# Performance work log

Measured on AMD Instinct MI355X. Metric: run time of the kernel, lower is better.

Reference implementation:

```python
import jax, jax.numpy as jnp
import numpy as np

EPS = 1e-3  # Keras LayerNormalization default epsilon


def _lstm(x, mask, Wk, Wr, b):
    """Masked Keras-style LSTM, return_sequences=True, zero initial state.
    x: [B,T,F], mask: [B,T] bool, Wk: [F,4U], Wr: [U,4U], b: [4U].
    Gate order i,f,g,o (Keras). Masked steps carry previous h,c through."""
    B, T, _ = x.shape
    U = Wr.shape[0]
    # precompute input projections for all timesteps: [B,T,4U]
    zx = jnp.einsum('btf,fg->btg', x, Wk) + b

    def step(carry, inp):
        h, c = carry
        zx_t, m_t = inp  # [B,4U], [B]
        z = zx_t + h @ Wr
        i, f, g, o = jnp.split(z, 4, axis=-1)
        c_new = jax.nn.sigmoid(f) * c + jax.nn.sigmoid(i) * jnp.tanh(g)
        h_new = jax.nn.sigmoid(o) * jnp.tanh(c_new)
        m = m_t[:, None]
        h = jnp.where(m, h_new, h)
        c = jnp.where(m, c_new, c)
        return (h, c), h

    init = (jnp.zeros((B, U), x.dtype), jnp.zeros((B, U), x.dtype))
    _, hs = jax.lax.scan(step, init, (jnp.swapaxes(zx, 0, 1), mask.T))
    return jnp.swapaxes(hs, 0, 1)  # [B,T,U]


def _layer_norm(x, gamma, beta):
    mu = jnp.mean(x, axis=-1, keepdims=True)
    var = jnp.var(x, axis=-1, keepdims=True)
    return (x - mu) * jax.lax.rsqrt(var + EPS) * gamma + beta


def setup_inputs() -> dict:
    key = jax.random.key(0)
    B, T, F, U, C = 128, 512, 3, 512, 5
    ks = jax.random.split(key, 12)
    s = 0.05
    inputs = jax.random.normal(ks[0], (B, T, F), dtype=jnp.float32)
    lengths = jax.random.randint(ks[1], (B,), T // 4, T + 1)
    masks = jnp.arange(T)[None, :] < lengths[:, None]  # [B,T] bool
    return {
        'inputs': inputs,
        'masks': masks,
        'Wk0': jax.random.normal(ks[2], (F, 4 * U), jnp.float32) * s,
        'Wr0': jax.random.normal(ks[3], (U, 4 * U), jnp.float32) * s,
        'b0': jnp.zeros((4 * U,), jnp.float32),
        'Wk1': jax.random.normal(ks[4], (U, 4 * U), jnp.float32) * s,
        'Wr1': jax.random.normal(ks[5], (U, 4 * U), jnp.float32) * s,
        'b1': jnp.zeros((4 * U,), jnp.float32),
        'gamma': jnp.ones((U,), jnp.float32),
        'beta': jnp.zeros((U,), jnp.float32),
        'Wfc': jax.random.normal(ks[6], (U, C), jnp.float32) * s,
        'bfc': jnp.zeros((C,), jnp.float32),
    }


def reference(inputs, masks, Wk0, Wr0, b0, Wk1, Wr1, b1, gamma, beta, Wfc, bfc):
    m = masks.astype(bool)
    h0 = _lstm(inputs, m, Wk0, Wr0, b0)
    h0 = _layer_norm(h0, gamma, beta)          # shared norm layer
    h1 = _lstm(h0, m, Wk1, Wr1, b1)
    h1 = _layer_norm(h1, gamma, beta)          # same gamma/beta reused
    logits = jnp.einsum('btu,uc->btc', h1, Wfc) + bfc
    return jax.nn.softmax(logits, axis=-1)     # [B,T,C]
```

## Files before the change

### kernel.cpp

```cpp
#include <hip/hip_runtime.h>
#include <stdint.h>

typedef _Float16 v8hf __attribute__((ext_vector_type(8)));
typedef float v4f __attribute__((ext_vector_type(4)));
typedef unsigned long long u64t;

static __device__ __forceinline__ uint16_t f2h(float f){ _Float16 h=(_Float16)f; uint16_t u; __builtin_memcpy(&u,&h,2); return u; }
static __device__ __forceinline__ float h2f(uint16_t u){ _Float16 h; __builtin_memcpy(&h,&u,2); return (float)h; }
static __device__ __forceinline__ float fsig(float x){ return __builtin_amdgcn_rcpf(1.f + __expf(-x)); }
static __device__ __forceinline__ float ftanh(float x){ return 2.f*__builtin_amdgcn_rcpf(1.f + __expf(-2.f*x)) - 1.f; }

#define P0OFF  65536
#define P1OFF  81920
#define MSOFF  98304
#define B1OFF  98560
#define LDSSZ  98944

__device__ __forceinline__ v4f quad_transpose(v4f v, int p) {
#pragma unroll
    for (int a = 1; a < 4; ++a) {
        v4f t;
#pragma unroll
        for (int j = 0; j < 4; ++j) t[j] = __shfl_xor(v[j ^ a], a);
#pragma unroll
        for (int j = 0; j < 4; ++j) if ((p ^ j) == a) v[j] = t[j];
    }
    return v;
}

__device__ __forceinline__ void stage_both(const uint16_t* __restrict__ s0,
                                           const uint16_t* __restrict__ s1,
                                           char* sm, float* muS, float* rsS, int doP1) {
    const int tid = threadIdx.x;
    const int lane = tid & 63;
    const u64t* a = (const u64t*)s0;
    const u64t* b = (const u64t*)s1;
    u64t va[8], vb[8];
#pragma unroll
    for (int i = 0; i < 4; ++i) {
        int c = 2 * (i * 256 + tid);
        va[2*i]   = __hip_atomic_load(a + c,     __ATOMIC_RELAXED, __HIP_MEMORY_SCOPE_AGENT);
        va[2*i+1] = __hip_atomic_load(a + c + 1, __ATOMIC_RELAXED, __HIP_MEMORY_SCOPE_AGENT);
    }
    if (doP1) {
#pragma unroll
        for (int i = 0; i < 4; ++i) {
            int c = 2 * (i * 256 + tid);
            vb[2*i]   = __hip_atomic_load(b + c,     __ATOMIC_RELAXED, __HIP_MEMORY_SCOPE_AGENT);
            vb[2*i+1] = __hip_atomic_load(b + c + 1, __ATOMIC_RELAXED, __HIP_MEMORY_SCOPE_AGENT);
        }
    }
#pragma unroll
    for (int i = 0; i < 4; ++i) {
        float ps = 0.f, pq = 0.f;
#pragma unroll
        for (int k = 0; k < 2; ++k) {
            u64t w = va[2*i + k];
#pragma unroll
            for (int h = 0; h < 4; ++h) {
                float f = h2f((uint16_t)(w >> (16*h)));
                ps += f; pq += f * f;
            }
        }
#pragma unroll
        for (int m = 1; m < 64; m <<= 1) { ps += __shfl_xor(ps, m); pq += __shfl_xor(pq, m); }
        int byte = (i * 256 + tid) << 4;
        int row = byte >> 10;
        if (lane == 0) {
            float mu = ps * (1.f / 512.f);
            muS[row] = mu;
            rsS[row] = rsqrtf(pq * (1.f / 512.f) - mu * mu + 1e-3f);
        }
        int sb = byte ^ ((row & 7) << 4);
        uint4 u;
        u.x = (unsigned)va[2*i];   u.y = (unsigned)(va[2*i]   >> 32);
        u.z = (unsigned)va[2*i+1]; u.w = (unsigned)(va[2*i+1] >> 32);
        *(uint4*)(sm + P0OFF + sb) = u;
        if (doP1) {
            uint4 v;
            v.x = (unsigned)vb[2*i];   v.y = (unsigned)(vb[2*i]   >> 32);
            v.z = (unsigned)vb[2*i+1]; v.w = (unsigned)(vb[2*i+1] >> 32);
            *(uint4*)(sm + P1OFF + sb) = v;
        }
    }
}

__global__ __launch_bounds__(64) void setup_lens(const void* mask, int* lens, int* gmax) {
    int b = blockIdx.x;
    int lane = threadIdx.x;
    const unsigned char* mp = (const unsigned char*)mask;
    int isbyte = (mp[1] != 0);
    int cnt = 0;
    if (isbyte) {
        const unsigned char* row = mp + (size_t)b * 512;
        for (int i = lane; i < 512; i += 64) cnt += (row[i] != 0) ? 1 : 0;
    } else {
        const int* row = ((const int*)mask) + (size_t)b * 512;
        for (int i = lane; i < 512; i += 64) cnt += (row[i] != 0) ? 1 : 0;
    }
#pragma unroll
    for (int off = 32; off > 0; off >>= 1) cnt += __shfl_down(cnt, off);
    if (lane == 0) { lens[b] = cnt; atomicMax(&gmax[b >> 4], cnt); }
}

__global__ __launch_bounds__(256, 1) void lstm_merged(
    const float* __restrict__ x, const float* __restrict__ Wk0, const float* __restrict__ Wr0,
    const float* __restrict__ b0, const float* __restrict__ Wk1, const float* __restrict__ Wr1,
    const float* __restrict__ b1, const float* __restrict__ gamma, const float* __restrict__ beta,
    const int* __restrict__ lens, const int* __restrict__ gmax,
    unsigned* __restrict__ slots, uint16_t* __restrict__ h0buf, uint16_t* __restrict__ h1hist)
{
    extern __shared__ char sm[];
    const int tid = threadIdx.x;
    const int lane = tid & 63;
    const int wv = tid >> 6;
    const int g  = blockIdx.x & 7;
    const int cs = blockIdx.x >> 3;
    const int u0 = cs << 4;

    const int rr = lane & 15;
    const int kb = (lane >> 4) << 3;

    for (int idx = tid; idx < 512 * 64; idx += 256) {
        int k = idx >> 6, j = idx & 63;
        size_t col = ((size_t)(j & 3) << 9) + u0 + ((j >> 4) << 2) + ((j >> 2) & 3);
        float v = Wr0[(size_t)k * 2048 + col];
        int byte = ((j << 10) + (k << 1)) ^ ((j & 7) << 4);
        *(uint16_t*)(sm + byte) = f2h(v);
    }
    for (int i = tid; i < 8192; i += 256) ((uint32_t*)(sm + P0OFF))[i] = 0u;
    float* muS = (float*)(sm + MSOFF);
    float* rsS = muS + 16;
    if (tid < 16) { muS[tid] = 0.f; rsS[tid] = rsqrtf(1e-3f); }

    v8hf wR[16], wK[16];
    {
        const size_t col = ((size_t)(rr & 3) << 9) + u0 + (wv << 2) + ((rr >> 2) & 3);
        float sb = 0.f;
#pragma unroll
        for (int kk = 0; kk < 16; ++kk) {
#pragma unroll
            for (int j = 0; j < 8; ++j) {
                int k = (kk << 5) + kb + j;
                float wr = Wr1[(size_t)k * 2048 + col];
                float wk = Wk1[(size_t)k * 2048 + col];
                wR[kk][j] = (_Float16)wr;
                wK[kk][j] = (_Float16)(gamma[k] * wk);
                sb += beta[k] * wk;
            }
        }
        sb += __shfl_xor(sb, 16); sb += __shfl_xor(sb, 32);
        if (lane < 16)
            ((float*)(sm + B1OFF))[(wv << 4) + lane] = b1[col] + sb;
    }

    const int row = ((lane >> 4) << 2) + (lane & 3);
    const int ul  = (lane >> 2) & 3;
    const int myu = u0 + (wv << 2) + ul;
    float wk0r[12], b0r[4], b1r[4];
#pragma unroll
    for (int G = 0; G < 4; ++G) {
#pragma unroll
        for (int f = 0; f < 3; ++f) wk0r[f * 4 + G] = Wk0[(size_t)f * 2048 + (G << 9) + myu];
        b0r[G] = b0[(G << 9) + myu];
    }
    __syncthreads();
#pragma unroll
    for (int G = 0; G < 4; ++G)
        b1r[G] = ((const float*)(sm + B1OFF))[(wv << 4) + (ul << 2) + G];

    const int len_row = lens[(g << 4) + row];
    const int ml = gmax[g];
    unsigned* slotg = slots + (g << 9);
    uint16_t* hh = h1hist + (size_t)g * 4194304;
    float c0 = 0.f, c1 = 0.f, ph0 = 0.f, ph1 = 0.f;
    const int lp = lane & 3;
    float px0, px1, px2;
    { const float* xp = x + ((size_t)((g << 4) + row) * 512) * 3;
      px0 = xp[0]; px1 = xp[1]; px2 = xp[2]; }
    __syncthreads();

    for (int t = 0;; ++t) {
        const float mu_r = muS[rr], rs_r = rsS[rr];
        const _Float16 rsh = (_Float16)rs_r;
        const _Float16 mrsh = (_Float16)(-mu_r * rs_r);
        v8hf rs8, mrs8;
#pragma unroll
        for (int j = 0; j < 8; ++j) { rs8[j] = rsh; mrs8[j] = mrsh; }
        v4f acc0 = {0,0,0,0}, accK = {0,0,0,0}, accR = {0,0,0,0};
#pragma unroll
        for (int kk = 0; kk < 16; ++kk) {
            int k = kb + (kk << 5);
            int ab = ((rr << 10) + (k << 1)) ^ ((rr & 7) << 4);
            v8hf a0 = *(const v8hf*)(sm + P0OFF + ab);
            int jr = (wv << 4) + rr;
            int bb = ((jr << 10) + (k << 1)) ^ ((jr & 7) << 4);
            v8hf bf = *(const v8hf*)(sm + bb);
            acc0 = __builtin_amdgcn_mfma_f32_16x16x32_f16(a0, bf, acc0, 0, 0, 0);
            v8hf an = a0 * rs8 + mrs8;
            accK = __builtin_amdgcn_mfma_f32_16x16x32_f16(an, wK[kk], accK, 0, 0, 0);
            v8hf a1 = *(const v8hf*)(sm + P1OFF + ab);
            accR = __builtin_amdgcn_mfma_f32_16x16x32_f16(a1, wR[kk], accR, 0, 0, 0);
        }
        v4f z0 = quad_transpose(acc0, lp);
        v4f z1 = quad_transpose(accR + accK, lp);
        __syncthreads();

        const u64t slotbase = (size_t)((((t + 1) & 1) << 3) + g) * 8192;
        if (t < ml) {
            float zg[4];
#pragma unroll
            for (int G = 0; G < 4; ++G)
                zg[G] = z0[G] + px0 * wk0r[G] + px1 * wk0r[4 + G] + px2 * wk0r[8 + G] + b0r[G];
            float si = fsig(zg[0]), sf = fsig(zg[1]);
            float tg = ftanh(zg[2]), so = fsig(zg[3]);
            float cn = sf * c0 + si * tg;
            float hn = so * ftanh(cn);
            if (t < len_row) c0 = cn; else hn = ph0;
            ph0 = hn;
            unsigned hu = f2h(hn);
            unsigned x4 = __shfl_xor(hu, 4);
            unsigned lo = ((lane & 4) == 0) ? (hu | (x4 << 16)) : (x4 | (hu << 16));
            unsigned hi = __shfl_xor(lo, 8);
            u64t v = ((lane & 8) == 0) ? ((u64t)lo | ((u64t)hi << 32)) : ((u64t)hi | ((u64t)lo << 32));
            if ((lane & 12) == 0)
                __hip_atomic_store((u64t*)(h0buf + slotbase + (row << 9) + u0 + (wv << 2)), v,
                                   __ATOMIC_RELAXED, __HIP_MEMORY_SCOPE_AGENT);
        }
        if (t >= 1) {
            float zg[4];
#pragma unroll
            for (int G = 0; G < 4; ++G) zg[G] = z1[G] + b1r[G];
            float si = fsig(zg[0]), sf = fsig(zg[1]);
            float tg = ftanh(zg[2]), so = fsig(zg[3]);
            float cn = sf * c1 + si * tg;
            float hn = so * ftanh(cn);
            if (t - 1 < len_row) c1 = cn; else hn = ph1;
            ph1 = hn;
            unsigned hu = f2h(hn);
            unsigned x4 = __shfl_xor(hu, 4);
            unsigned lo = ((lane & 4) == 0) ? (hu | (x4 << 16)) : (x4 | (hu << 16));
            unsigned hi = __shfl_xor(lo, 8);
            u64t v = ((lane & 8) == 0) ? ((u64t)lo | ((u64t)hi << 32)) : ((u64t)hi | ((u64t)lo << 32));
            if ((lane & 12) == 0)
                *(u64t*)(hh + (size_t)(t - 1) * 8192 + (row << 9) + u0 + (wv << 2)) = v;
        }
        if (t == ml) break;
        __syncthreads();

        if (tid == 0)
            __hip_atomic_fetch_add(slotg + (cs << 4), 1u,
                                   __ATOMIC_RELAXED, __HIP_MEMORY_SCOPE_AGENT);
        { int tn = (t + 1 < ml) ? t + 1 : ml - 1;
          const float* xp = x + ((size_t)((g << 4) + row) * 512 + tn) * 3;
          px0 = xp[0]; px1 = xp[1]; px2 = xp[2]; }
        if (tid < 32) {
            const unsigned tgt = (unsigned)(t + 1);
            const unsigned* sp = slotg + (tid << 4);
            long guard = 0;
            for (;;) {
                unsigned v = __hip_atomic_load(sp, __ATOMIC_RELAXED, __HIP_MEMORY_SCOPE_AGENT);
                if ((__ballot(v >= tgt) & 0xFFFFFFFFull) == 0xFFFFFFFFull) break;
                __builtin_amdgcn_s_sleep(1);
                if (++guard > 300000L) break;
            }
        }
        __syncthreads();
        stage_both(h0buf + (size_t)((((t + 1) & 1) << 3) + g) * 8192,
                   hh + (size_t)(t >= 1 ? t - 1 : 0) * 8192,
                   sm, muS, rsS, t >= 1);
        __syncthreads();
    }
}

__global__ __launch_bounds__(256) void finalize(
    const uint16_t* __restrict__ h1hist, const int* __restrict__ gmax,
    const float* __restrict__ gamma, const float* __restrict__ beta,
    const float* __restrict__ Wfc, const float* __restrict__ bfc,
    float* __restrict__ out)
{
    int wv = threadIdx.x >> 6, lane = threadIdx.x & 63;
    int rid = blockIdx.x * 4 + wv;
    int b = rid >> 9, t = rid & 511;
    int g = b >> 4, r = b & 15;
    int ml = gmax[g];
    int ts = t < ml ? t : ml - 1;
    const uint16_t* hp = h1hist + (size_t)g * 4194304 + (size_t)ts * 8192 + (r << 9) + (lane << 3);
    v8hf h8 = *(const v8hf*)hp;
    float hv[8]; float s = 0.f, q2 = 0.f;
#pragma unroll
    for (int j = 0; j < 8; ++j) { float f = (float)h8[j]; hv[j] = f; s += f; q2 += f * f; }
#pragma unroll
    for (int m = 1; m < 64; m <<= 1) { s += __shfl_xor(s, m); q2 += __shfl_xor(q2, m); }
    float mu = s * (1.f / 512.f);
    float rstd = rsqrtf(q2 * (1.f / 512.f) - mu * mu + 1e-3f);
    float p0=0,p1=0,p2=0,p3=0,p4=0;
#pragma unroll
    for (int j = 0; j < 8; ++j) {
        int k = (lane << 3) + j;
        float hn = (hv[j] - mu) * rstd * gamma[k] + beta[k];
        const float* wf = Wfc + (size_t)k * 5;
        p0 += hn*wf[0]; p1 += hn*wf[1]; p2 += hn*wf[2]; p3 += hn*wf[3]; p4 += hn*wf[4];
    }
#pragma unroll
    for (int m = 1; m < 64; m <<= 1) {
        p0 += __shfl_xor(p0,m); p1 += __shfl_xor(p1,m); p2 += __shfl_xor(p2,m);
        p3 += __shfl_xor(p3,m); p4 += __shfl_xor(p4,m);
    }
    if (lane == 0) {
        float l0=p0+bfc[0], l1=p1+bfc[1], l2=p2+bfc[2], l3=p3+bfc[3], l4=p4+bfc[4];
        float mx = fmaxf(fmaxf(fmaxf(l0,l1),fmaxf(l2,l3)),l4);
        float e0=__expf(l0-mx), e1=__expf(l1-mx), e2=__expf(l2-mx), e3=__expf(l3-mx), e4=__expf(l4-mx);
        float inv = 1.f/(e0+e1+e2+e3+e4);
        float* op = out + (size_t)rid * 5;
        op[0]=e0*inv; op[1]=e1*inv; op[2]=e2*inv; op[3]=e3*inv; op[4]=e4*inv;
    }
}

extern "C" void kernel_launch(void* const* d_in, const int* in_sizes, int n_in,
                              void* d_out, int out_size, void* d_ws, size_t ws_size,
                              hipStream_t stream) {
    (void)in_sizes; (void)n_in; (void)out_size;
    const float* x     = (const float*)d_in[0];
    const void*  mask  = d_in[1];
    const float* Wk0   = (const float*)d_in[2];
    const float* Wr0   = (const float*)d_in[3];
    const float* b0    = (const float*)d_in[4];
    const float* Wk1   = (const float*)d_in[5];
    const float* Wr1   = (const float*)d_in[6];
    const float* b1    = (const float*)d_in[7];
    const float* gamma = (const float*)d_in[8];
    const float* beta  = (const float*)d_in[9];
    const float* Wfc   = (const float*)d_in[10];
    const float* bfc   = (const float*)d_in[11];
    float* out = (float*)d_out;
    char* ws = (char*)d_ws;
    unsigned* slots  = (unsigned*)(ws);
    int*      lens   = (int*)(ws + 16384);
    int*      gmax   = (int*)(ws + 16896);
    uint16_t* h0buf  = (uint16_t*)(ws + 32768);
    uint16_t* h1hist = (uint16_t*)(ws + 294912);
    if (ws_size < 67403776) return;

    hipFuncSetAttribute((const void*)lstm_merged, hipFuncAttributeMaxDynamicSharedMemorySize, LDSSZ);
    hipMemsetAsync(ws, 0, 32768, stream);
    setup_lens<<<128, 64, 0, stream>>>(mask, lens, gmax);
    lstm_merged<<<256, 256, LDSSZ, stream>>>(x, Wk0, Wr0, b0, Wk1, Wr1, b1, gamma, beta,
                                             lens, gmax, slots, h0buf, h1hist);
    finalize<<<16384, 256, 0, stream>>>(h1hist, gmax, gamma, beta, Wfc, bfc, out);
}
```

Baseline: 2.646 ms.

## Split layer0/layer1 sync into separate counters with double-buffered h0 staging

Replaces the single per-step grid barrier with two independent counter sets, one for layer-0 and one for layer-1 hidden states. Each block now aggregates its release through an LDS counter, and layer 1 reads history from two steps back instead of one. The h0 staging buffer and its LayerNorm stats are double-buffered so that layer-0 publishing and layer-1 polling can decouple and overlap. The intent is to cut barrier wait on the recurrent critical path. The cost is more LDS use and more intricate ordering, with some risk of correctness issues such as the t-2 history lag and an LDS atomic counter being read without a fence.

```diff
diff --git a/kernel.cpp b/kernel.cpp
--- a/kernel.cpp
+++ b/kernel.cpp
@@ -10,11 +10,13 @@
 static __device__ __forceinline__ float fsig(float x){ return __builtin_amdgcn_rcpf(1.f + __expf(-x)); }
 static __device__ __forceinline__ float ftanh(float x){ return 2.f*__builtin_amdgcn_rcpf(1.f + __expf(-2.f*x)) - 1.f; }
 
-#define P0OFF  65536
-#define P1OFF  81920
-#define MSOFF  98304
-#define B1OFF  98560
-#define LDSSZ  98944
+#define P0AOFF 65536
+#define P1OFF  98304
+#define MSOFF  114688
+#define B1OFF  114944
+#define CT0OFF 115200
+#define CT1OFF 115204
+#define LDSSZ  115264
 
 __device__ __forceinline__ v4f quad_transpose(v4f v, int p) {
 #pragma unroll
@@ -26,63 +28,6 @@
         for (int j = 0; j < 4; ++j) if ((p ^ j) == a) v[j] = t[j];
     }
     return v;
-}
-
-__device__ __forceinline__ void stage_both(const uint16_t* __restrict__ s0,
-                                           const uint16_t* __restrict__ s1,
-                                           char* sm, float* muS, float* rsS, int doP1) {
-    const int tid = threadIdx.x;
-    const int lane = tid & 63;
-    const u64t* a = (const u64t*)s0;
-    const u64t* b = (const u64t*)s1;
-    u64t va[8], vb[8];
-#pragma unroll
-    for (int i = 0; i < 4; ++i) {
-        int c = 2 * (i * 256 + tid);
-        va[2*i]   = __hip_atomic_load(a + c,     __ATOMIC_RELAXED, __HIP_MEMORY_SCOPE_AGENT);
-        va[2*i+1] = __hip_atomic_load(a + c + 1, __ATOMIC_RELAXED, __HIP_MEMORY_SCOPE_AGENT);
-    }
-    if (doP1) {
-#pragma unroll
-        for (int i = 0; i < 4; ++i) {
-            int c = 2 * (i * 256 + tid);
-            vb[2*i]   = __hip_atomic_load(b + c,     __ATOMIC_RELAXED, __HIP_MEMORY_SCOPE_AGENT);
-            vb[2*i+1] = __hip_atomic_load(b + c + 1, __ATOMIC_RELAXED, __HIP_MEMORY_SCOPE_AGENT);
-        }
-    }
-#pragma unroll
-    for (int i = 0; i < 4; ++i) {
-        float ps = 0.f, pq = 0.f;
-#pragma unroll
-        for (int k = 0; k < 2; ++k) {
-            u64t w = va[2*i + k];
-#pragma unroll
-            for (int h = 0; h < 4; ++h) {
-                float f = h2f((uint16_t)(w >> (16*h)));
-                ps += f; pq += f * f;
-            }
-        }
-#pragma unroll
-        for (int m = 1; m < 64; m <<= 1) { ps += __shfl_xor(ps, m); pq += __shfl_xor(pq, m); }
-        int byte = (i * 256 + tid) << 4;
-        int row = byte >> 10;
-        if (lane == 0) {
-            float mu = ps * (1.f / 512.f);
-            muS[row] = mu;
-            rsS[row] = rsqrtf(pq * (1.f / 512.f) - mu * mu + 1e-3f);
-        }
-        int sb = byte ^ ((row & 7) << 4);
-        uint4 u;
-        u.x = (unsigned)va[2*i];   u.y = (unsigned)(va[2*i]   >> 32);
-        u.z = (unsigned)va[2*i+1]; u.w = (unsigned)(va[2*i+1] >> 32);
-        *(uint4*)(sm + P0OFF + sb) = u;
-        if (doP1) {
-            uint4 v;
-            v.x = (unsigned)vb[2*i];   v.y = (unsigned)(vb[2*i]   >> 32);
-            v.z = (unsigned)vb[2*i+1]; v.w = (unsigned)(vb[2*i+1] >> 32);
-            *(uint4*)(sm + P1OFF + sb) = v;
-        }
-    }
 }
 
 __global__ __launch_bounds__(64) void setup_lens(const void* mask, int* lens, int* gmax) {
@@ -101,6 +46,29 @@
 #pragma unroll
     for (int off = 32; off > 0; off >>= 1) cnt += __shfl_down(cnt, off);
     if (lane == 0) { lens[b] = cnt; atomicMax(&gmax[b >> 4], cnt); }
+}
+
+__device__ __forceinline__ void poll32(const unsigned* slotbase, unsigned tgt, int lane) {
+    const unsigned* sp = slotbase + ((lane & 31) << 4);
+    long guard = 0;
+    for (;;) {
+        unsigned v = (lane < 32)
+            ? __hip_atomic_load(sp, __ATOMIC_RELAXED, __HIP_MEMORY_SCOPE_AGENT)
+            : 0xFFFFFFFFu;
+        if (__ballot(v >= tgt) == ~0ull) break;
+        __builtin_amdgcn_s_sleep(1);
+        if (++guard > 150000L) break;
+    }
+}
+
+__device__ __forceinline__ void agg_release(char* sm, int ctroff, unsigned epoch_t,
+                                            unsigned* gslot, int lane) {
+    asm volatile("s_waitcnt vmcnt(0)" ::: "memory");
+    if (lane == 0) {
+        unsigned old = atomicAdd((unsigned*)(sm + ctroff), 1u);
+        if (old == 4u * epoch_t + 3u)
+            __hip_atomic_fetch_add(gslot, 1u, __ATOMIC_RELAXED, __HIP_MEMORY_SCOPE_AGENT);
+    }
 }
 
 __global__ __launch_bounds__(256, 1) void lstm_merged(
@@ -128,10 +96,12 @@
         int byte = ((j << 10) + (k << 1)) ^ ((j & 7) << 4);
         *(uint16_t*)(sm + byte) = f2h(v);
     }
-    for (int i = tid; i < 8192; i += 256) ((uint32_t*)(sm + P0OFF))[i] = 0u;
-    float* muS = (float*)(sm + MSOFF);
-    float* rsS = muS + 16;
-    if (tid < 16) { muS[tid] = 0.f; rsS[tid] = rsqrtf(1e-3f); }
+    for (int i = tid; i < 12288; i += 256) ((uint32_t*)(sm + P0AOFF))[i] = 0u;
+    if (tid < 16) {
+        ((float*)(sm + MSOFF))[tid] = 0.f;       ((float*)(sm + MSOFF))[16 + tid] = rsqrtf(1e-3f);
+        ((float*)(sm + MSOFF + 128))[tid] = 0.f; ((float*)(sm + MSOFF + 128))[16 + tid] = rsqrtf(1e-3f);
+    }
+    if (tid == 0) { *(unsigned*)(sm + CT0OFF) = 0u; *(unsigned*)(sm + CT1OFF) = 0u; }
 
     v8hf wR[16], wK[16];
     {
@@ -171,7 +141,8 @@
 
     const int len_row = lens[(g << 4) + row];
     const int ml = gmax[g];
-    unsigned* slotg = slots + (g << 9);
+    unsigned* slot0g = slots + (g << 10);
+    unsigned* slot1g = slot0g + 512;
     uint16_t* hh = h1hist + (size_t)g * 4194304;
     float c0 = 0.f, c1 = 0.f, ph0 = 0.f, ph1 = 0.f;
     const int lp = lane & 3;
@@ -181,33 +152,32 @@
     __syncthreads();
 
     for (int t = 0;; ++t) {
-        const float mu_r = muS[rr], rs_r = rsS[rr];
+        const int par = t & 1;
+        const char* p0base = sm + P0AOFF + (par << 14);
+        const float* muSp = (const float*)(sm + MSOFF + (par << 7));
+
+        const float mu_r = muSp[rr], rs_r = muSp[16 + rr];
         const _Float16 rsh = (_Float16)rs_r;
         const _Float16 mrsh = (_Float16)(-mu_r * rs_r);
         v8hf rs8, mrs8;
 #pragma unroll
         for (int j = 0; j < 8; ++j) { rs8[j] = rsh; mrs8[j] = mrsh; }
-        v4f acc0 = {0,0,0,0}, accK = {0,0,0,0}, accR = {0,0,0,0};
+        v4f acc0 = {0,0,0,0}, accK = {0,0,0,0};
 #pragma unroll
         for (int kk = 0; kk < 16; ++kk) {
             int k = kb + (kk << 5);
             int ab = ((rr << 10) + (k << 1)) ^ ((rr & 7) << 4);
-            v8hf a0 = *(const v8hf*)(sm + P0OFF + ab);
+            v8hf a0 = *(const v8hf*)(p0base + ab);
             int jr = (wv << 4) + rr;
             int bb = ((jr << 10) + (k << 1)) ^ ((jr & 7) << 4);
             v8hf bf = *(const v8hf*)(sm + bb);
             acc0 = __builtin_amdgcn_mfma_f32_16x16x32_f16(a0, bf, acc0, 0, 0, 0);
             v8hf an = a0 * rs8 + mrs8;
             accK = __builtin_amdgcn_mfma_f32_16x16x32_f16(an, wK[kk], accK, 0, 0, 0);
-            v8hf a1 = *(const v8hf*)(sm + P1OFF + ab);
-            accR = __builtin_amdgcn_mfma_f32_16x16x32_f16(a1, wR[kk], accR, 0, 0, 0);
-        }
-        v4f z0 = quad_transpose(acc0, lp);
-        v4f z1 = quad_transpose(accR + accK, lp);
-        __syncthreads();
-
-        const u64t slotbase = (size_t)((((t + 1) & 1) << 3) + g) * 8192;
+        }
+
         if (t < ml) {
+            v4f z0 = quad_transpose(acc0, lp);
             float zg[4];
 #pragma unroll
             for (int G = 0; G < 4; ++G)
@@ -223,11 +193,46 @@
             unsigned lo = ((lane & 4) == 0) ? (hu | (x4 << 16)) : (x4 | (hu << 16));
             unsigned hi = __shfl_xor(lo, 8);
             u64t v = ((lane & 8) == 0) ? ((u64t)lo | ((u64t)hi << 32)) : ((u64t)hi | ((u64t)lo << 32));
+            size_t sb = (size_t)((((t + 1) & 1) << 3) + g) * 8192;
             if ((lane & 12) == 0)
-                __hip_atomic_store((u64t*)(h0buf + slotbase + (row << 9) + u0 + (wv << 2)), v,
+                __hip_atomic_store((u64t*)(h0buf + sb + (row << 9) + u0 + (wv << 2)), v,
                                    __ATOMIC_RELAXED, __HIP_MEMORY_SCOPE_AGENT);
+            agg_release(sm, CT0OFF, (unsigned)t, slot0g + (cs << 4), lane);
+        }
+
+        if (t >= 2) {
+            poll32(slot1g, (unsigned)t, lane);
+            const u64t* src = (const u64t*)(hh + (size_t)(t - 2) * 8192);
+            u64t w[8];
+#pragma unroll
+            for (int i = 0; i < 4; ++i) {
+                int c = 2 * (i * 256 + tid);
+                w[2*i]   = __hip_atomic_load(src + c,     __ATOMIC_RELAXED, __HIP_MEMORY_SCOPE_AGENT);
+                w[2*i+1] = __hip_atomic_load(src + c + 1, __ATOMIC_RELAXED, __HIP_MEMORY_SCOPE_AGENT);
+            }
+#pragma unroll
+            for (int i = 0; i < 4; ++i) {
+                int byte = (i * 256 + tid) << 4;
+                int r2 = byte >> 10;
+                int sbz = byte ^ ((r2 & 7) << 4);
+                uint4 u;
+                u.x = (unsigned)w[2*i];   u.y = (unsigned)(w[2*i]   >> 32);
+                u.z = (unsigned)w[2*i+1]; u.w = (unsigned)(w[2*i+1] >> 32);
+                *(uint4*)(sm + P1OFF + sbz) = u;
+            }
+        }
+        __syncthreads();
+
+        v4f accR = {0,0,0,0};
+#pragma unroll
+        for (int kk = 0; kk < 16; ++kk) {
+            int k = kb + (kk << 5);
+            int ab = ((rr << 10) + (k << 1)) ^ ((rr & 7) << 4);
+            v8hf a1 = *(const v8hf*)(sm + P1OFF + ab);
+            accR = __builtin_amdgcn_mfma_f32_16x16x32_f16(a1, wR[kk], accR, 0, 0, 0);
         }
         if (t >= 1) {
+            v4f z1 = quad_transpose(accK + accR, lp);
             float zg[4];
 #pragma unroll
             for (int G = 0; G < 4; ++G) zg[G] = z1[G] + b1r[G];
@@ -246,29 +251,52 @@
                 *(u64t*)(hh + (size_t)(t - 1) * 8192 + (row << 9) + u0 + (wv << 2)) = v;
         }
         if (t == ml) break;
-        __syncthreads();
-
-        if (tid == 0)
-            __hip_atomic_fetch_add(slotg + (cs << 4), 1u,
-                                   __ATOMIC_RELAXED, __HIP_MEMORY_SCOPE_AGENT);
+        agg_release(sm, CT1OFF, (unsigned)t, slot1g + (cs << 4), lane);
+
         { int tn = (t + 1 < ml) ? t + 1 : ml - 1;
           const float* xp = x + ((size_t)((g << 4) + row) * 512 + tn) * 3;
           px0 = xp[0]; px1 = xp[1]; px2 = xp[2]; }
-        if (tid < 32) {
-            const unsigned tgt = (unsigned)(t + 1);
-            const unsigned* sp = slotg + (tid << 4);
-            long guard = 0;
-            for (;;) {
-                unsigned v = __hip_atomic_load(sp, __ATOMIC_RELAXED, __HIP_MEMORY_SCOPE_AGENT);
-                if ((__ballot(v >= tgt) & 0xFFFFFFFFull) == 0xFFFFFFFFull) break;
-                __builtin_amdgcn_s_sleep(1);
-                if (++guard > 300000L) break;
-            }
-        }
-        __syncthreads();
-        stage_both(h0buf + (size_t)((((t + 1) & 1) << 3) + g) * 8192,
-                   hh + (size_t)(t >= 1 ? t - 1 : 0) * 8192,
-                   sm, muS, rsS, t >= 1);
+
+        poll32(slot0g, (unsigned)(t + 1), lane);
+        {
+            const u64t* src = (const u64t*)(h0buf + (size_t)((((t + 1) & 1) << 3) + g) * 8192);
+            float* muN = (float*)(sm + MSOFF + ((par ^ 1) << 7));
+            char* p0n = sm + P0AOFF + ((par ^ 1) << 14);
+            u64t w[8];
+#pragma unroll
+            for (int i = 0; i < 4; ++i) {
+                int c = 2 * (i * 256 + tid);
+                w[2*i]   = __hip_atomic_load(src + c,     __ATOMIC_RELAXED, __HIP_MEMORY_SCOPE_AGENT);
+                w[2*i+1] = __hip_atomic_load(src + c + 1, __ATOMIC_RELAXED, __HIP_MEMORY_SCOPE_AGENT);
+            }
+#pragma unroll
+            for (int i = 0; i < 4; ++i) {
+                float ps = 0.f, pq = 0.f;
+#pragma unroll
+                for (int k = 0; k < 2; ++k) {
+                    u64t ww = w[2*i + k];
+#pragma unroll
+                    for (int h = 0; h < 4; ++h) {
+                        float f = h2f((uint16_t)(ww >> (16*h)));
+                        ps += f; pq += f * f;
+                    }
+                }
+#pragma unroll
+                for (int m = 1; m < 64; m <<= 1) { ps += __shfl_xor(ps, m); pq += __shfl_xor(pq, m); }
+                int byte = (i * 256 + tid) << 4;
+                int r2 = byte >> 10;
+                if (lane == 0) {
+                    float mu = ps * (1.f / 512.f);
+                    muN[r2] = mu;
+                    muN[16 + r2] = rsqrtf(pq * (1.f / 512.f) - mu * mu + 1e-3f);
+                }
+                int sbz = byte ^ ((r2 & 7) << 4);
+                uint4 u;
+                u.x = (unsigned)w[2*i];   u.y = (unsigned)(w[2*i]   >> 32);
+                u.z = (unsigned)w[2*i+1]; u.w = (unsigned)(w[2*i+1] >> 32);
+                *(uint4*)(p0n + sbz) = u;
+            }
+        }
         __syncthreads();
     }
 }
@@ -336,14 +364,14 @@
     float* out = (float*)d_out;
     char* ws = (char*)d_ws;
     unsigned* slots  = (unsigned*)(ws);
-    int*      lens   = (int*)(ws + 16384);
-    int*      gmax   = (int*)(ws + 16896);
-    uint16_t* h0buf  = (uint16_t*)(ws + 32768);
-    uint16_t* h1hist = (uint16_t*)(ws + 294912);
-    if (ws_size < 67403776) return;
+    int*      lens   = (int*)(ws + 32768);
+    int*      gmax   = (int*)(ws + 33280);
+    uint16_t* h0buf  = (uint16_t*)(ws + 36864);
+    uint16_t* h1hist = (uint16_t*)(ws + 299008);
+    if (ws_size < 67407872) return;
 
     hipFuncSetAttribute((const void*)lstm_merged, hipFuncAttributeMaxDynamicSharedMemorySize, LDSSZ);
-    hipMemsetAsync(ws, 0, 32768, stream);
+    hipMemsetAsync(ws, 0, 36864, stream);
     setup_lens<<<128, 64, 0, stream>>>(mask, lens, gmax);
     lstm_merged<<<256, 256, LDSSZ, stream>>>(x, Wk0, Wr0, b0, Wk1, Wr1, b1, gamma, beta,
                                              lens, gmax, slots, h0buf, h1hist);
```

After: 2.799 ms. +5.8%, slower.
